# Kernel optimization log

Hardware: AMD Instinct MI355X
Metric: run time of the kernel (lower is better)

Reference implementation:

```python
import jax, jax.numpy as jnp
import numpy as np

B, N, NC = 8, 25200, 80           # YOLOv5-640 / COCO raw output
CONF_THRES = 0.25                  # init conf_threshold
IOU_THRES = 0.45                   # init iou_threshold
PATCH_CONF = 0.001                 # hard-coded patch_conf in forward
GN = jnp.array([640.0, 640.0, 640.0, 640.0], dtype=jnp.float32)  # img_size[[1,0,1,0]]
MAX_WH = 4096.0                    # class offset for class-aware NMS
K_CLEAN = 512                      # fixed-size cap on NMS candidates (clean branch)
K_PATCH = 1024                     # fixed-size cap on NMS candidates (patch branch)
MAX_DET_CLEAN = 1000
MAX_DET_PATCH = 30000
NEG = jnp.float32(-1e30)


def _xywh2xyxy(x):
    xy, wh = x[..., :2], x[..., 2:4]
    return jnp.concatenate([xy - wh * 0.5, xy + wh * 0.5], axis=-1)


def _pairwise_iou(a, b):
    # a: [A,4] xyxy, b: [B,4] xyxy -> [A,B] jaccard overlap
    tl = jnp.maximum(a[:, None, :2], b[None, :, :2])
    br = jnp.minimum(a[:, None, 2:4], b[None, :, 2:4])
    wh = jnp.clip(br - tl, 0.0)
    inter = wh[..., 0] * wh[..., 1]
    area_a = (a[:, 2] - a[:, 0]) * (a[:, 3] - a[:, 1])
    area_b = (b[:, 2] - b[:, 0]) * (b[:, 3] - b[:, 1])
    union = area_a[:, None] + area_b[None, :] - inter
    union = jnp.where(union > 0, union, 1.0)  # guard degenerate boxes
    return inter / union


def _nms_single(pred, conf_thres, K, max_det):
    # pred: [N, 5+nc]. Fixed-size (padded/masked) greedy NMS, class-aware via MAX_WH offset.
    obj = pred[:, 4]
    cls_conf = pred[:, 5:] * obj[:, None]          # x[:,5:] *= x[:,4:5]
    conf = jnp.max(cls_conf, axis=-1)
    cls = jnp.argmax(cls_conf, axis=-1)
    box = _xywh2xyxy(pred[:, :4])
    valid = (obj > conf_thres) & (conf > conf_thres)
    scores = jnp.where(valid, conf, NEG)
    top_scores, idx = jax.lax.top_k(scores, K)     # sorted desc, like torchvision NMS ordering
    boxes = box[idx]
    cls_k = cls[idx]
    valid_k = top_scores > conf_thres
    boxes_off = boxes + cls_k.astype(boxes.dtype)[:, None] * MAX_WH
    iou = jax.lax.stop_gradient(_pairwise_iou(boxes_off, boxes_off))
    ar = jnp.arange(K)

    def step(keep, i):
        sup = keep[i] & (iou[i] > IOU_THRES) & (ar > i)
        return keep & (~sup), None

    keep, _ = jax.lax.scan(step, valid_k, jnp.arange(K))
    rank = jnp.cumsum(keep.astype(jnp.int32))
    keep = keep & (rank <= max_det)
    return boxes, cls_k, keep


def _image_loss(cb, cc, ck, pb, pc, pk):
    # per clean detection: max IoU over kept patch boxes of the same class (0 if none)
    iou = _pairwise_iou(cb / GN, pb / GN)          # [K_CLEAN, K_PATCH]
    mask = ck[:, None] & pk[None, :] & (cc[:, None] == pc[None, :])
    tm = jnp.max(jnp.where(mask, iou, 0.0), axis=1)
    s = jnp.sum(jnp.where(ck, tm, 0.0))
    n = jnp.sum(ck.astype(jnp.float32))
    return s, n


def _forward(output_clean, output_patch):
    cb, cc, ck = jax.vmap(lambda p: _nms_single(p, CONF_THRES, K_CLEAN, MAX_DET_CLEAN))(output_clean)
    pb, pc, pk = jax.vmap(lambda p: _nms_single(p, PATCH_CONF, K_PATCH, MAX_DET_PATCH))(output_patch)
    s, n = jax.vmap(_image_loss)(cb, cc, ck, pb, pc, pk)
    total, cnt = jnp.sum(s), jnp.sum(n)
    return jnp.where(cnt > 0, 1.0 - total / jnp.maximum(cnt, 1.0), jnp.float32(1.0))


def _make_pred(key):
    ka, kb, kc, kd = jax.random.split(key, 4)
    cxcy = jax.random.uniform(ka, (B, N, 2), jnp.float32, 20.0, 620.0)
    wh = jax.random.uniform(kb, (B, N, 2), jnp.float32, 2.0, 150.0)
    obj = jax.random.uniform(kc, (B, N, 1), jnp.float32)
    clsp = jax.random.uniform(kd, (B, N, NC), jnp.float32)
    return jnp.concatenate([cxcy, wh, obj, clsp], axis=-1)


def setup_inputs() -> dict:
    key = jax.random.key(0)
    k1, k2 = jax.random.split(key)
    return {"output_clean": _make_pred(k1), "output_patch": _make_pred(k2)}


def reference(output_clean, output_patch):
    return _forward(output_clean, output_patch)
```

## Files before the change

### kernel.cpp

```cpp
#include <hip/hip_runtime.h>


static constexpr int NB   = 8;
static constexpr int NA   = 25200;
static constexpr int NCLS = 80;
static constexpr int CH   = 85;
static constexpr int NT   = 16;
static constexpr int KMAX = 1024;
static constexpr int NBIN = 32768;
static constexpr int PSH  = 17;
static constexpr int CAP  = 2048;
static constexpr int IOB  = 34;

static constexpr size_t OFF_KEYS = 0;
static constexpr size_t OFF_CLS  = OFF_KEYS + (size_t)NT * NA * 4;
static constexpr size_t OFF_BOX  = OFF_CLS  + (size_t)NT * NA * 4;
static constexpr size_t OFF_CLSK = OFF_BOX  + (size_t)NT * KMAX * 16;
static constexpr size_t OFF_VALK = OFF_CLSK + (size_t)NT * KMAX * 4;
static constexpr size_t OFF_KEEP = OFF_VALK + (size_t)NT * KMAX * 4;
static constexpr size_t OFF_SUP  = OFF_KEEP + (size_t)NT * 16 * 8;
static constexpr size_t OFF_DIAG = OFF_SUP  + (size_t)NT * KMAX * 16 * 8;
static constexpr size_t OFF_PART = OFF_DIAG + (size_t)NT * KMAX * 8;

__device__ __forceinline__ unsigned okey(float f) {
  unsigned u = __float_as_uint(f);
  return (u & 0x80000000u) ? ~u : (u | 0x80000000u);
}

__device__ __forceinline__ unsigned long long shflx64(unsigned long long v, int m) {
  unsigned lo = (unsigned)v, hi = (unsigned)(v >> 32);
  lo = __shfl_xor(lo, m);
  hi = __shfl_xor(hi, m);
  return ((unsigned long long)hi << 32) | lo;
}

__global__ __launch_bounds__(256) void k_score(const float* __restrict__ clean,
                                               const float* __restrict__ patch,
                                               unsigned* __restrict__ keys,
                                               int* __restrict__ clsArr) {
#pragma clang fp contract(off)
  __shared__ float rows[4][16 * CH];
  const int t    = blockIdx.y;
  const int wave = threadIdx.x >> 6;
  const int lane = threadIdx.x & 63;
  const int a0   = blockIdx.x * 64 + wave * 16;
  if (a0 >= NA) return;
  const float conf_th = (t < 8) ? 0.25f : 0.001f;
  const float* __restrict__ src = ((t < 8) ? clean : patch) + (size_t)(t & 7) * NA * CH;
  const float4* g4 = (const float4*)(src + (size_t)a0 * CH);
  float4* rows4 = (float4*)rows[wave];
#pragma unroll
  for (int c = 0; c < 6; ++c) {
    const int i = (c << 6) + lane;
    if (i < 340) {
      __builtin_amdgcn_global_load_lds(
          (const __attribute__((address_space(1))) void*)(g4 + i),
          (__attribute__((address_space(3))) void*)(rows4 + (c << 6)),
          16, 0, 2 );
    }
  }
  asm volatile("s_waitcnt vmcnt(0)" ::: "memory");
  __builtin_amdgcn_sched_barrier(0);

  const int ar = lane >> 2;
  const int q  = lane & 3;
  const float* r = rows[wave] + ar * CH;
  const float obj = r[4];
  const int c0 = q * 20;
  float best = r[5 + c0] * obj;
  int bc = c0;
  for (int c = c0 + 1; c < c0 + 20; ++c) {
    float v = r[5 + c] * obj;
    if (v > best) { best = v; bc = c; }
  }
  {
    float b2 = __shfl_down(best, 2); int c2 = __shfl_down(bc, 2);
    if (b2 > best || (b2 == best && c2 < bc)) { best = b2; bc = c2; }
    float b1 = __shfl_down(best, 1); int c1 = __shfl_down(bc, 1);
    if (b1 > best || (b1 == best && c1 < bc)) { best = b1; bc = c1; }
  }
  if (q == 0) {
    const bool valid = (obj > conf_th) && (best > conf_th);
    const float score = valid ? best : -1e30f;
    const int a = a0 + ar;
    keys[(size_t)t * NA + a]   = okey(score);
    clsArr[(size_t)t * NA + a] = bc;
  }
}

__global__ __launch_bounds__(1024) void k_topsel(const unsigned* __restrict__ keys,
                                                 const int* __restrict__ clsArr,
                                                 const float* __restrict__ clean,
                                                 const float* __restrict__ patch,
                                                 float* __restrict__ boxesK,
                                                 int* __restrict__ clsK,
                                                 int* __restrict__ validK) {
#pragma clang fp contract(off)
  const int t = blockIdx.x;
  const unsigned K = (t < 8) ? 512u : 1024u;
  const float conf_th = (t < 8) ? 0.25f : 0.001f;
  __shared__ unsigned h32[NBIN / 2];
  __shared__ unsigned long long buf[CAP];
  __shared__ unsigned scnt[2];
  __shared__ unsigned wtot[16], wsuf[16];
  __shared__ int s_chunk;
  __shared__ unsigned s_acc, s_B;
  const int tid = threadIdx.x;
  const int lane = tid & 63, wv = tid >> 6;
  for (int i = tid; i < NBIN / 2; i += 1024) h32[i] = 0u;
  for (int i = tid; i < CAP; i += 1024) buf[i] = 0ull;
  if (tid < 2) scnt[tid] = 0u;
  __syncthreads();
  const unsigned INVKEY = okey(-1e30f);
  const unsigned* kv = keys + (size_t)t * NA;
  {
    const uint4* kv4 = (const uint4*)kv;
    unsigned invCnt = 0;
    for (int i = tid; i < NA / 4; i += 1024) {
      uint4 kq = kv4[i];
      unsigned kk[4] = {kq.x, kq.y, kq.z, kq.w};
#pragma unroll
      for (int c = 0; c < 4; ++c) {
        if (kk[c] == INVKEY) {
          ++invCnt;
        } else {
          unsigned b = kk[c] >> PSH;
          atomicAdd(&h32[b >> 1], 1u << ((b & 1) * 16));
        }
      }
    }
    for (int off = 32; off > 0; off >>= 1) invCnt += __shfl_down(invCnt, off);
    if (lane == 0 && invCnt) {
      unsigned b = INVKEY >> PSH;
      atomicAdd(&h32[b >> 1], invCnt << ((b & 1) * 16));
    }
  }
  __syncthreads();
  unsigned cnt_c = 0;
  for (int i = 0; i < 16; ++i) {
    unsigned v = h32[tid * 16 + i];
    cnt_c += (v & 0xFFFFu) + (v >> 16);
  }
  unsigned s = cnt_c;
  for (int off = 1; off < 64; off <<= 1) {
    unsigned v = __shfl_down(s, off);
    if (lane + off < 64) s += v;
  }
  if (lane == 0) wtot[wv] = s;
  __syncthreads();
  if (tid < 16) {
    unsigned acc = 0;
    for (int w2 = 15; w2 > tid; --w2) acc += wtot[w2];
    wsuf[tid] = acc;
  }
  __syncthreads();
  const unsigned suf = s + wsuf[wv];
  if (suf >= K && suf - cnt_c < K) { s_chunk = tid; s_acc = suf - cnt_c; }
  __syncthreads();
  if (tid == 0) {
    unsigned acc = s_acc;
    unsigned res = (unsigned)(s_chunk * 32);
    for (int i = 31; i >= 0; --i) {
      int bb = s_chunk * 32 + i;
      unsigned v = h32[bb >> 1];
      unsigned c2 = (bb & 1) ? (v >> 16) : (v & 0xFFFFu);
      if (acc + c2 >= K) { res = (unsigned)bb; break; }
      acc += c2;
    }
    s_B = res;
  }
  __syncthreads();
  const unsigned B = s_B;
  const unsigned long long lowmask =
      (lane == 0) ? 0ull : (0xFFFFFFFFFFFFFFFFull >> (64 - lane));
  for (int i = tid; i < 25600; i += 1024) {
    const bool inb = (i < NA);
    unsigned key = inb ? kv[i] : 0u;
    unsigned p = key >> PSH;
    const bool hi = inb && (p > B);
    const bool eq = inb && (p == B);
    const unsigned long long item =
        ((unsigned long long)key << 32) | (unsigned)(~(unsigned)i);
    unsigned long long mh = __ballot(hi);
    if (mh) {
      int leader = (int)__ffsll(mh) - 1;
      unsigned base2 = 0;
      if (lane == leader) base2 = atomicAdd(&scnt[0], (unsigned)__popcll(mh));
      base2 = __shfl(base2, leader);
      if (hi) {
        unsigned pos = base2 + (unsigned)__popcll(mh & lowmask);
        if (pos < 1024u) buf[pos] = item;
      }
    }
    unsigned long long me = __ballot(eq);
    if (me) {
      int leader = (int)__ffsll(me) - 1;
      unsigned base2 = 0;
      if (lane == leader) base2 = atomicAdd(&scnt[1], (unsigned)__popcll(me));
      base2 = __shfl(base2, leader);
      if (eq) {
        unsigned pos = base2 + (unsigned)__popcll(me & lowmask);
        if (pos < 1024u) buf[1024 + pos] = item;
      }
    }
  }
  __syncthreads();
  {
    const int e0 = wv * 128 + lane;
    const int e1 = e0 + 64;
    unsigned long long r0 = buf[e0], r1 = buf[e1];
    for (int kk2 = 2; kk2 <= CAP; kk2 <<= 1) {
      for (int j = kk2 >> 1; j > 0; j >>= 1) {
        if (j >= 128) {
          buf[e0] = r0; buf[e1] = r1;
          __syncthreads();
          unsigned long long o0 = buf[e0 ^ j];
          unsigned long long o1 = buf[e1 ^ j];
          const bool mx = (((e0 & kk2) == 0) == ((e0 & j) == 0));
          r0 = mx ? (r0 > o0 ? r0 : o0) : (r0 < o0 ? r0 : o0);
          r1 = mx ? (r1 > o1 ? r1 : o1) : (r1 < o1 ? r1 : o1);
          __syncthreads();
        } else if (j == 64) {
          const bool up = (e0 & kk2) == 0;
          unsigned long long mxv = r0 > r1 ? r0 : r1;
          unsigned long long mnv = r0 > r1 ? r1 : r0;
          r0 = up ? mxv : mnv;
          r1 = up ? mnv : mxv;
        } else {
          unsigned long long o0 = shflx64(r0, j);
          unsigned long long o1 = shflx64(r1, j);
          const bool up0 = (e0 & kk2) == 0;
          const bool up1 = (e1 & kk2) == 0;
          const bool lo  = (lane & j) == 0;
          const bool m0 = (up0 == lo), m1 = (up1 == lo);
          r0 = m0 ? (r0 > o0 ? r0 : o0) : (r0 < o0 ? r0 : o0);
          r1 = m1 ? (r1 > o1 ? r1 : o1) : (r1 < o1 ? r1 : o1);
        }
      }
    }
    buf[e0] = r0; buf[e1] = r1;
  }
  __syncthreads();
  const float* __restrict__ src = ((t < 8) ? clean : patch) + (size_t)(t & 7) * NA * CH;
  const unsigned vkey = okey(conf_th);
  for (int k = tid; k < (int)K; k += 1024) {
    unsigned long long v = buf[k];
    unsigned key = (unsigned)(v >> 32);
    int idx = (int)(~(unsigned)(v & 0xFFFFFFFFull));
    if (idx < 0 || idx >= NA) idx = 0;
    const float* r = src + (size_t)idx * CH;
    float cx = r[0], cy = r[1], w = r[2], h = r[3];
    float hw = w * 0.5f, hh = h * 0.5f;
    float* bo = boxesK + ((size_t)t * KMAX + k) * 4;
    bo[0] = cx - hw; bo[1] = cy - hh; bo[2] = cx + hw; bo[3] = cy + hh;
    clsK[t * KMAX + k]   = clsArr[(size_t)t * NA + idx];
    validK[t * KMAX + k] = (key > vkey) ? 1 : 0;
  }
}

__global__ __launch_bounds__(256) void k_ioumat(const float* __restrict__ boxesK,
                                                const int* __restrict__ clsK,
                                                unsigned long long* __restrict__ sup,
                                                unsigned long long* __restrict__ diag) {
#pragma clang fp contract(off)
  const int t  = blockIdx.y;
  const int K  = (t < 8) ? 512 : 1024;
  const int lw = (t < 8) ? 3 : 4;
  const int nw = 1 << lw;
  const int npair = (nw * (nw + 1)) / 2;
  const int total = npair * 64;
  if (blockIdx.x * 256 >= total) return;
  __shared__ float X1[KMAX + 16], Y1[KMAX + 16], X2[KMAX + 16], Y2[KMAX + 16], AR[KMAX + 16];
  for (int i = threadIdx.x; i < K; i += 256) {
    const float* bo = boxesK + ((size_t)t * KMAX + i) * 4;
    float off = (float)clsK[t * KMAX + i] * 4096.0f;
    float x1 = bo[0] + off, y1 = bo[1] + off, x2 = bo[2] + off, y2 = bo[3] + off;
    const int ip = i + (i >> 6);
    X1[ip] = x1; Y1[ip] = y1; X2[ip] = x2; Y2[ip] = y2;
    AR[ip] = (x2 - x1) * (y2 - y1);
  }
  __syncthreads();
  unsigned long long* supt = sup + (size_t)t * (KMAX * 16);
  for (int widx = blockIdx.x * 256 + threadIdx.x; widx < total; widx += IOB * 256) {
    int p = widx >> 6;
    int row = widx & 63;
    int rb = 0, pr = p;
    while (pr >= nw - rb) { pr -= nw - rb; ++rb; }
    const int wc = rb + pr;
    const int i = rb * 64 + row;
    const int ipi = i + rb;
    const float x1i = X1[ipi], y1i = Y1[ipi], x2i = X2[ipi], y2i = Y2[ipi], ai = AR[ipi];
    unsigned long long m = 0ull;
    const int jb = (wc << 6) + wc;
    const bool offd = (wc > rb);
#pragma unroll 4
    for (int l = 0; l < 64; ++l) {
      const int jp = jb + l;
      float tlx = fmaxf(x1i, X1[jp]);
      float tly = fmaxf(y1i, Y1[jp]);
      float brx = fminf(x2i, X2[jp]);
      float bry = fminf(y2i, Y2[jp]);
      float w = fmaxf(brx - tlx, 0.0f);
      float h = fmaxf(bry - tly, 0.0f);
      float inter = w * h;
      float uni = (ai + AR[jp]) - inter;
      uni = (uni > 0.0f) ? uni : 1.0f;
      float iou = inter / uni;
      bool hit = (iou > 0.45f) && (offd || ((wc << 6) + l > i));
      m |= hit ? (1ull << l) : 0ull;
    }
    supt[(size_t)i * nw + wc] = m;
    if (wc == rb) diag[(size_t)t * KMAX + i] = m;
  }
}

__global__ __launch_bounds__(64) void k_greedy(const unsigned long long* __restrict__ sup,
                                               const unsigned long long* __restrict__ diag,
                                               const int* __restrict__ validK,
                                               unsigned long long* __restrict__ keepw) {
  const int t  = blockIdx.x;
  const int K  = (t < 8) ? 512 : 1024;
  const int lw = (t < 8) ? 3 : 4;
  const int nw = 1 << lw;
  const int lane = threadIdx.x;
  __shared__ unsigned long long sdiag[KMAX];
  const unsigned long long* dg = diag + (size_t)t * KMAX;
  for (int i = lane; i < K; i += 64) sdiag[i] = dg[i];
  int v16[16];
#pragma unroll
  for (int W = 0; W < 16; ++W)
    v16[W] = (W < nw) ? validK[t * KMAX + W * 64 + lane] : 0;
  unsigned long long vkeep = 0ull;
#pragma unroll
  for (int W = 0; W < 16; ++W)
    if (W < nw) {
      unsigned long long bl = __ballot(v16[W] != 0);
      if (lane == W) vkeep = bl;
    }
  __syncthreads();
  const int w = lane & (nw - 1);
  const int b = lane >> lw;
  const int r0 = b * nw;
  const unsigned long long* base = sup + (size_t)t * (KMAX * 16);
  unsigned long long remv = 0ull;
  for (int W = 0; W < nw; ++W) {
    unsigned long long vv[16];
    if (W + 1 < nw) {
#pragma unroll
      for (int j = 0; j < 16; ++j)
        vv[j] = (j < nw) ? base[(size_t)(W * 64 + r0 + j) * nw + w] : 0ull;
    }
    unsigned long long cur = __shfl(vkeep, W) & ~__shfl(remv, W);
    for (int rb = 0; rb < 64; rb += 16) {
      unsigned long long tm[16];
#pragma unroll
      for (int i2 = 0; i2 < 16; ++i2) tm[i2] = sdiag[W * 64 + rb + i2];
#pragma unroll
      for (int i2 = 0; i2 < 16; ++i2) {
        unsigned long long msk = 0ull - ((cur >> (rb + i2)) & 1ull);
        cur &= ~(tm[i2] & msk);
      }
    }
    if (lane == 0) keepw[t * 16 + W] = cur;
    if (W + 1 < nw) {
      unsigned long long part = 0ull;
#pragma unroll
      for (int j = 0; j < 16; ++j) {
        bool take = (j < nw) && (w > W) && ((cur >> (r0 + j)) & 1ull);
        part |= take ? vv[j] : 0ull;
      }
      for (int s = nw; s < 64; s <<= 1) part |= __shfl_xor(part, s);
      remv |= part;
    }
  }
}

__global__ __launch_bounds__(1024) void k_loss(const float* __restrict__ boxesK,
                                               const int* __restrict__ clsK,
                                               const unsigned long long* __restrict__ keepw,
                                               float* __restrict__ part) {
#pragma clang fp contract(off)
  const int img = blockIdx.y;
  const int chunk = blockIdx.x;
  const int tp = 8 + img;
  __shared__ float px1[KMAX], py1[KMAX], px2[KMAX], py2[KMAX], pa[KMAX];
  __shared__ int pcls[KMAX];
  __shared__ float red[1024];
  for (int j = threadIdx.x; j < KMAX; j += 1024) {
    const float* bo = boxesK + ((size_t)tp * KMAX + j) * 4;
    float x1 = bo[0] / 640.0f, y1 = bo[1] / 640.0f;
    float x2 = bo[2] / 640.0f, y2 = bo[3] / 640.0f;
    px1[j] = x1; py1[j] = y1; px2[j] = x2; py2[j] = y2;
    pa[j] = (x2 - x1) * (y2 - y1);
    int kept = (int)((keepw[tp * 16 + (j >> 6)] >> (j & 63)) & 1ull);
    pcls[j] = kept ? clsK[tp * KMAX + j] : -1;
  }
  __syncthreads();
  const int row = chunk * 64 + (threadIdx.x & 63);
  const int stripe = threadIdx.x >> 6;
  const int ck = (int)((keepw[img * 16 + (row >> 6)] >> (row & 63)) & 1ull);
  const float* bo = boxesK + ((size_t)img * KMAX + row) * 4;
  float cx1 = bo[0] / 640.0f, cy1 = bo[1] / 640.0f;
  float cx2 = bo[2] / 640.0f, cy2 = bo[3] / 640.0f;
  float ca = (cx2 - cx1) * (cy2 - cy1);
  const int ccls = clsK[img * KMAX + row];
  float m = 0.0f;
  if (ck) {
    const int j0 = stripe * 64;
    for (int j = j0; j < j0 + 64; ++j) {
      if (pcls[j] == ccls) {
        float tlx = fmaxf(cx1, px1[j]);
        float tly = fmaxf(cy1, py1[j]);
        float brx = fminf(cx2, px2[j]);
        float bry = fminf(cy2, py2[j]);
        float w = fmaxf(brx - tlx, 0.0f);
        float h = fmaxf(bry - tly, 0.0f);
        float inter = w * h;
        float uni = (ca + pa[j]) - inter;
        uni = (uni > 0.0f) ? uni : 1.0f;
        m = fmaxf(m, inter / uni);
      }
    }
  }
  red[threadIdx.x] = m;
  __syncthreads();
  if (threadIdx.x < 64) {
    float mm = red[threadIdx.x];
#pragma unroll
    for (int s = 1; s < 16; ++s) mm = fmaxf(mm, red[threadIdx.x + 64 * s]);
    float sv = ck ? mm : 0.0f;
    float nv = ck ? 1.0f : 0.0f;
    for (int off = 32; off > 0; off >>= 1) {
      sv += __shfl_down(sv, off);
      nv += __shfl_down(nv, off);
    }
    if (threadIdx.x == 0) {
      int b = img * 8 + chunk;
      part[b * 2 + 0] = sv;
      part[b * 2 + 1] = nv;
    }
  }
}

__global__ __launch_bounds__(64) void k_final(const float* __restrict__ part,
                                              float* __restrict__ out) {
  int lane = threadIdx.x;
  float sv = part[lane * 2 + 0];
  float nv = part[lane * 2 + 1];
  for (int off = 32; off > 0; off >>= 1) {
    sv += __shfl_down(sv, off);
    nv += __shfl_down(nv, off);
  }
  if (lane == 0) out[0] = (nv > 0.0f) ? (1.0f - sv / fmaxf(nv, 1.0f)) : 1.0f;
}

extern "C" void kernel_launch(void* const* d_in, const int* in_sizes, int n_in,
                              void* d_out, int out_size, void* d_ws, size_t ws_size,
                              hipStream_t stream) {
  const float* clean = (const float*)d_in[0];
  const float* patch = (const float*)d_in[1];
  char* ws = (char*)d_ws;
  unsigned* keys            = (unsigned*)(ws + OFF_KEYS);
  int* clsArr               = (int*)(ws + OFF_CLS);
  float* boxesK             = (float*)(ws + OFF_BOX);
  int* clsK                 = (int*)(ws + OFF_CLSK);
  int* validK               = (int*)(ws + OFF_VALK);
  unsigned long long* keepw = (unsigned long long*)(ws + OFF_KEEP);
  unsigned long long* sup   = (unsigned long long*)(ws + OFF_SUP);
  unsigned long long* diag  = (unsigned long long*)(ws + OFF_DIAG);
  float* part               = (float*)(ws + OFF_PART);
  float* out                = (float*)d_out;

  k_score  <<<dim3((NA + 63) / 64, NT), 256, 0, stream>>>(clean, patch, keys, clsArr);
  k_topsel <<<NT, 1024, 0, stream>>>(keys, clsArr, clean, patch, boxesK, clsK, validK);
  k_ioumat <<<dim3(IOB, NT), 256, 0, stream>>>(boxesK, clsK, sup, diag);
  k_greedy <<<NT, 64, 0, stream>>>(sup, diag, validK, keepw);
  k_loss   <<<dim3(8, NB), 1024, 0, stream>>>(boxesK, clsK, keepw, part);
  k_final  <<<1, 64, 0, stream>>>(part, out);
}
```

Before: 247.9 us.

## Build score histogram with global atomics in scoring kernel instead of top-select

Moves the per-task radix histogram construction out of the single-block-per-task top-select kernel and into the massively parallel scoring kernel, which now does global atomic adds into a workspace histogram zeroed by a new kernel. The top-select kernel loads its histogram slice into registers, finds the threshold bin without shared memory, and keeps the keys in registers for the compaction pass instead of reading them again. This removes the serial shared-memory histogram phase done by only 16 blocks. In exchange it adds a zeroing launch, global atomic contention on hot bins (the invalid-key bin is aggregated per wave), and higher register pressure.

```diff
diff --git a/kernel.cpp b/kernel.cpp
--- a/kernel.cpp
+++ b/kernel.cpp
@@ -21,6 +21,7 @@
 static constexpr size_t OFF_SUP  = OFF_KEEP + (size_t)NT * 16 * 8;
 static constexpr size_t OFF_DIAG = OFF_SUP  + (size_t)NT * KMAX * 16 * 8;
 static constexpr size_t OFF_PART = OFF_DIAG + (size_t)NT * KMAX * 8;
+static constexpr size_t OFF_HIST = OFF_PART + 512;
 
 __device__ __forceinline__ unsigned okey(float f) {
   unsigned u = __float_as_uint(f);
@@ -34,10 +35,15 @@
   return ((unsigned long long)hi << 32) | lo;
 }
 
+__global__ __launch_bounds__(256) void k_zero(uint4* __restrict__ hist4) {
+  hist4[blockIdx.x * 256 + threadIdx.x] = make_uint4(0u, 0u, 0u, 0u);
+}
+
 __global__ __launch_bounds__(256) void k_score(const float* __restrict__ clean,
                                                const float* __restrict__ patch,
                                                unsigned* __restrict__ keys,
-                                               int* __restrict__ clsArr) {
+                                               int* __restrict__ clsArr,
+                                               unsigned* __restrict__ hist) {
 #pragma clang fp contract(off)
   __shared__ float rows[4][16 * CH];
   const int t    = blockIdx.y;
@@ -82,9 +88,18 @@
   if (q == 0) {
     const bool valid = (obj > conf_th) && (best > conf_th);
     const float score = valid ? best : -1e30f;
+    const unsigned key = okey(score);
     const int a = a0 + ar;
-    keys[(size_t)t * NA + a]   = okey(score);
+    keys[(size_t)t * NA + a]   = key;
     clsArr[(size_t)t * NA + a] = bc;
+    unsigned* ht = hist + (size_t)t * NBIN;
+    if (valid) {
+      atomicAdd(&ht[key >> PSH], 1u);
+    } else {
+      unsigned long long mb = __ballot(true);
+      if (lane == (int)__ffsll(mb) - 1)
+        atomicAdd(&ht[okey(-1e30f) >> PSH], (unsigned)__popcll(mb));
+    }
   }
 }
 
@@ -92,6 +107,7 @@
                                                  const int* __restrict__ clsArr,
                                                  const float* __restrict__ clean,
                                                  const float* __restrict__ patch,
+                                                 const unsigned* __restrict__ hist,
                                                  float* __restrict__ boxesK,
                                                  int* __restrict__ clsK,
                                                  int* __restrict__ validK) {
@@ -99,48 +115,35 @@
   const int t = blockIdx.x;
   const unsigned K = (t < 8) ? 512u : 1024u;
   const float conf_th = (t < 8) ? 0.25f : 0.001f;
-  __shared__ unsigned h32[NBIN / 2];
   __shared__ unsigned long long buf[CAP];
   __shared__ unsigned scnt[2];
   __shared__ unsigned wtot[16], wsuf[16];
-  __shared__ int s_chunk;
-  __shared__ unsigned s_acc, s_B;
+  __shared__ unsigned s_B;
   const int tid = threadIdx.x;
   const int lane = tid & 63, wv = tid >> 6;
-  for (int i = tid; i < NBIN / 2; i += 1024) h32[i] = 0u;
   for (int i = tid; i < CAP; i += 1024) buf[i] = 0ull;
   if (tid < 2) scnt[tid] = 0u;
-  __syncthreads();
-  const unsigned INVKEY = okey(-1e30f);
   const unsigned* kv = keys + (size_t)t * NA;
+  const uint4* kv4 = (const uint4*)kv;
+  uint4 u[7];
+#pragma unroll
+  for (int c = 0; c < 7; ++c) {
+    const int i4 = c * 1024 + tid;
+    if (i4 < NA / 4) u[c] = kv4[i4];
+    else { u[c].x = 0u; u[c].y = 0u; u[c].z = 0u; u[c].w = 0u; }
+  }
+  unsigned hb[32];
   {
-    const uint4* kv4 = (const uint4*)kv;
-    unsigned invCnt = 0;
-    for (int i = tid; i < NA / 4; i += 1024) {
-      uint4 kq = kv4[i];
-      unsigned kk[4] = {kq.x, kq.y, kq.z, kq.w};
-#pragma unroll
-      for (int c = 0; c < 4; ++c) {
-        if (kk[c] == INVKEY) {
-          ++invCnt;
-        } else {
-          unsigned b = kk[c] >> PSH;
-          atomicAdd(&h32[b >> 1], 1u << ((b & 1) * 16));
-        }
-      }
-    }
-    for (int off = 32; off > 0; off >>= 1) invCnt += __shfl_down(invCnt, off);
-    if (lane == 0 && invCnt) {
-      unsigned b = INVKEY >> PSH;
-      atomicAdd(&h32[b >> 1], invCnt << ((b & 1) * 16));
-    }
-  }
-  __syncthreads();
+    const uint4* gh4 = (const uint4*)(hist + (size_t)t * NBIN + (size_t)tid * 32);
+#pragma unroll
+    for (int i = 0; i < 8; ++i) {
+      uint4 h4 = gh4[i];
+      hb[i * 4 + 0] = h4.x; hb[i * 4 + 1] = h4.y; hb[i * 4 + 2] = h4.z; hb[i * 4 + 3] = h4.w;
+    }
+  }
   unsigned cnt_c = 0;
-  for (int i = 0; i < 16; ++i) {
-    unsigned v = h32[tid * 16 + i];
-    cnt_c += (v & 0xFFFFu) + (v >> 16);
-  }
+#pragma unroll
+  for (int i = 0; i < 32; ++i) cnt_c += hb[i];
   unsigned s = cnt_c;
   for (int off = 1; off < 64; off <<= 1) {
     unsigned v = __shfl_down(s, off);
@@ -155,17 +158,17 @@
   }
   __syncthreads();
   const unsigned suf = s + wsuf[wv];
-  if (suf >= K && suf - cnt_c < K) { s_chunk = tid; s_acc = suf - cnt_c; }
-  __syncthreads();
-  if (tid == 0) {
-    unsigned acc = s_acc;
-    unsigned res = (unsigned)(s_chunk * 32);
+  if (suf >= K && suf - cnt_c < K) {
+    unsigned acc = suf - cnt_c;
+    unsigned res = (unsigned)(tid * 32);
+    bool found = false;
+#pragma unroll
     for (int i = 31; i >= 0; --i) {
-      int bb = s_chunk * 32 + i;
-      unsigned v = h32[bb >> 1];
-      unsigned c2 = (bb & 1) ? (v >> 16) : (v & 0xFFFFu);
-      if (acc + c2 >= K) { res = (unsigned)bb; break; }
-      acc += c2;
+      const unsigned c2 = hb[i];
+      if (!found) {
+        if (acc + c2 >= K) { res = (unsigned)(tid * 32 + i); found = true; }
+        else acc += c2;
+      }
     }
     s_B = res;
   }
@@ -173,34 +176,41 @@
   const unsigned B = s_B;
   const unsigned long long lowmask =
       (lane == 0) ? 0ull : (0xFFFFFFFFFFFFFFFFull >> (64 - lane));
-  for (int i = tid; i < 25600; i += 1024) {
-    const bool inb = (i < NA);
-    unsigned key = inb ? kv[i] : 0u;
-    unsigned p = key >> PSH;
-    const bool hi = inb && (p > B);
-    const bool eq = inb && (p == B);
-    const unsigned long long item =
-        ((unsigned long long)key << 32) | (unsigned)(~(unsigned)i);
-    unsigned long long mh = __ballot(hi);
-    if (mh) {
-      int leader = (int)__ffsll(mh) - 1;
-      unsigned base2 = 0;
-      if (lane == leader) base2 = atomicAdd(&scnt[0], (unsigned)__popcll(mh));
-      base2 = __shfl(base2, leader);
-      if (hi) {
-        unsigned pos = base2 + (unsigned)__popcll(mh & lowmask);
-        if (pos < 1024u) buf[pos] = item;
-      }
-    }
-    unsigned long long me = __ballot(eq);
-    if (me) {
-      int leader = (int)__ffsll(me) - 1;
-      unsigned base2 = 0;
-      if (lane == leader) base2 = atomicAdd(&scnt[1], (unsigned)__popcll(me));
-      base2 = __shfl(base2, leader);
-      if (eq) {
-        unsigned pos = base2 + (unsigned)__popcll(me & lowmask);
-        if (pos < 1024u) buf[1024 + pos] = item;
+#pragma unroll
+  for (int c = 0; c < 7; ++c) {
+    const int i4 = c * 1024 + tid;
+    const bool inb = (i4 < NA / 4);
+    unsigned kk[4] = {u[c].x, u[c].y, u[c].z, u[c].w};
+#pragma unroll
+    for (int e = 0; e < 4; ++e) {
+      const unsigned key = kk[e];
+      const unsigned p = key >> PSH;
+      const bool hi = inb && (p > B);
+      const bool eq = inb && (p == B);
+      const int idx = i4 * 4 + e;
+      const unsigned long long item =
+          ((unsigned long long)key << 32) | (unsigned)(~(unsigned)idx);
+      unsigned long long mh = __ballot(hi);
+      if (mh) {
+        int leader = (int)__ffsll(mh) - 1;
+        unsigned base2 = 0;
+        if (lane == leader) base2 = atomicAdd(&scnt[0], (unsigned)__popcll(mh));
+        base2 = __shfl(base2, leader);
+        if (hi) {
+          unsigned pos = base2 + (unsigned)__popcll(mh & lowmask);
+          if (pos < 1024u) buf[pos] = item;
+        }
+      }
+      unsigned long long me = __ballot(eq);
+      if (me) {
+        int leader = (int)__ffsll(me) - 1;
+        unsigned base2 = 0;
+        if (lane == leader) base2 = atomicAdd(&scnt[1], (unsigned)__popcll(me));
+        base2 = __shfl(base2, leader);
+        if (eq) {
+          unsigned pos = base2 + (unsigned)__popcll(me & lowmask);
+          if (pos < 1024u) buf[1024 + pos] = item;
+        }
       }
     }
   }
@@ -469,10 +479,12 @@
   unsigned long long* sup   = (unsigned long long*)(ws + OFF_SUP);
   unsigned long long* diag  = (unsigned long long*)(ws + OFF_DIAG);
   float* part               = (float*)(ws + OFF_PART);
+  unsigned* hist            = (unsigned*)(ws + OFF_HIST);
   float* out                = (float*)d_out;
 
-  k_score  <<<dim3((NA + 63) / 64, NT), 256, 0, stream>>>(clean, patch, keys, clsArr);
-  k_topsel <<<NT, 1024, 0, stream>>>(keys, clsArr, clean, patch, boxesK, clsK, validK);
+  k_zero   <<<(NT * NBIN * 4) / (16 * 256), 256, 0, stream>>>((uint4*)hist);
+  k_score  <<<dim3((NA + 63) / 64, NT), 256, 0, stream>>>(clean, patch, keys, clsArr, hist);
+  k_topsel <<<NT, 1024, 0, stream>>>(keys, clsArr, clean, patch, hist, boxesK, clsK, validK);
   k_ioumat <<<dim3(IOB, NT), 256, 0, stream>>>(boxesK, clsK, sup, diag);
   k_greedy <<<NT, 64, 0, stream>>>(sup, diag, validK, keepw);
   k_loss   <<<dim3(8, NB), 1024, 0, stream>>>(boxesK, clsK, keepw, part);
```

Measured after the change: 316.5 us. 1.28x slower.

## Fuse final reduction into loss kernel and double rows per scoring wave

Applied to the files above, without the earlier changes.

The final reduction kernel is removed. The last k_loss block to finish, detected through an atomic counter that k_score resets, now performs the 64-way reduction and writes the output, saving one kernel launch. k_score also processes 32 anchors per wave instead of 16, with two lanes per anchor scanning 40 classes each, which halves the grid size and doubles the LDS staging per wave. The costs are longer serial argmax loops per lane and reliance on threadfence and atomic ordering for correctness.

```diff
diff --git a/kernel.cpp b/kernel.cpp
--- a/kernel.cpp
+++ b/kernel.cpp
@@ -21,6 +21,7 @@
 static constexpr size_t OFF_SUP  = OFF_KEEP + (size_t)NT * 16 * 8;
 static constexpr size_t OFF_DIAG = OFF_SUP  + (size_t)NT * KMAX * 16 * 8;
 static constexpr size_t OFF_PART = OFF_DIAG + (size_t)NT * KMAX * 8;
+static constexpr size_t OFF_CNT  = OFF_PART + 512;
 
 __device__ __forceinline__ unsigned okey(float f) {
   unsigned u = __float_as_uint(f);
@@ -37,22 +38,26 @@
 __global__ __launch_bounds__(256) void k_score(const float* __restrict__ clean,
                                                const float* __restrict__ patch,
                                                unsigned* __restrict__ keys,
-                                               int* __restrict__ clsArr) {
+                                               int* __restrict__ clsArr,
+                                               unsigned* __restrict__ cnt) {
 #pragma clang fp contract(off)
-  __shared__ float rows[4][16 * CH];
+  if (blockIdx.x == 0 && blockIdx.y == 0 && threadIdx.x == 0) *cnt = 0u;
+  __shared__ float rows[4][32 * CH];
   const int t    = blockIdx.y;
   const int wave = threadIdx.x >> 6;
   const int lane = threadIdx.x & 63;
-  const int a0   = blockIdx.x * 64 + wave * 16;
+  const int a0   = blockIdx.x * 128 + wave * 32;
   if (a0 >= NA) return;
+  const int nA = (NA - a0 < 32) ? (NA - a0) : 32;
   const float conf_th = (t < 8) ? 0.25f : 0.001f;
   const float* __restrict__ src = ((t < 8) ? clean : patch) + (size_t)(t & 7) * NA * CH;
   const float4* g4 = (const float4*)(src + (size_t)a0 * CH);
   float4* rows4 = (float4*)rows[wave];
-#pragma unroll
-  for (int c = 0; c < 6; ++c) {
+  const int n4 = (nA * CH) >> 2;
+#pragma unroll
+  for (int c = 0; c < 11; ++c) {
     const int i = (c << 6) + lane;
-    if (i < 340) {
+    if (i < n4) {
       __builtin_amdgcn_global_load_lds(
           (const __attribute__((address_space(1))) void*)(g4 + i),
           (__attribute__((address_space(3))) void*)(rows4 + (c << 6)),
@@ -62,29 +67,27 @@
   asm volatile("s_waitcnt vmcnt(0)" ::: "memory");
   __builtin_amdgcn_sched_barrier(0);
 
-  const int ar = lane >> 2;
-  const int q  = lane & 3;
-  const float* r = rows[wave] + ar * CH;
-  const float obj = r[4];
-  const int c0 = q * 20;
-  float best = r[5 + c0] * obj;
-  int bc = c0;
-  for (int c = c0 + 1; c < c0 + 20; ++c) {
-    float v = r[5 + c] * obj;
-    if (v > best) { best = v; bc = c; }
-  }
-  {
-    float b2 = __shfl_down(best, 2); int c2 = __shfl_down(bc, 2);
-    if (b2 > best || (b2 == best && c2 < bc)) { best = b2; bc = c2; }
+  const int ar = lane >> 1;
+  const int q  = lane & 1;
+  if (ar < nA) {
+    const float* r = rows[wave] + ar * CH;
+    const float obj = r[4];
+    const int c0 = q * 40;
+    float best = r[5 + c0] * obj;
+    int bc = c0;
+    for (int c = c0 + 1; c < c0 + 40; ++c) {
+      float v = r[5 + c] * obj;
+      if (v > best) { best = v; bc = c; }
+    }
     float b1 = __shfl_down(best, 1); int c1 = __shfl_down(bc, 1);
     if (b1 > best || (b1 == best && c1 < bc)) { best = b1; bc = c1; }
-  }
-  if (q == 0) {
-    const bool valid = (obj > conf_th) && (best > conf_th);
-    const float score = valid ? best : -1e30f;
-    const int a = a0 + ar;
-    keys[(size_t)t * NA + a]   = okey(score);
-    clsArr[(size_t)t * NA + a] = bc;
+    if (q == 0) {
+      const bool valid = (obj > conf_th) && (best > conf_th);
+      const float score = valid ? best : -1e30f;
+      const int a = a0 + ar;
+      keys[(size_t)t * NA + a]   = okey(score);
+      clsArr[(size_t)t * NA + a] = bc;
+    }
   }
 }
 
@@ -378,7 +381,9 @@
 __global__ __launch_bounds__(1024) void k_loss(const float* __restrict__ boxesK,
                                                const int* __restrict__ clsK,
                                                const unsigned long long* __restrict__ keepw,
-                                               float* __restrict__ part) {
+                                               float* __restrict__ part,
+                                               unsigned* __restrict__ cnt,
+                                               float* __restrict__ out) {
 #pragma clang fp contract(off)
   const int img = blockIdx.y;
   const int chunk = blockIdx.x;
@@ -386,6 +391,7 @@
   __shared__ float px1[KMAX], py1[KMAX], px2[KMAX], py2[KMAX], pa[KMAX];
   __shared__ int pcls[KMAX];
   __shared__ float red[1024];
+  __shared__ unsigned s_last;
   for (int j = threadIdx.x; j < KMAX; j += 1024) {
     const float* bo = boxesK + ((size_t)tp * KMAX + j) * 4;
     float x1 = bo[0] / 640.0f, y1 = bo[1] / 640.0f;
@@ -438,20 +444,23 @@
       int b = img * 8 + chunk;
       part[b * 2 + 0] = sv;
       part[b * 2 + 1] = nv;
-    }
-  }
-}
-
-__global__ __launch_bounds__(64) void k_final(const float* __restrict__ part,
-                                              float* __restrict__ out) {
-  int lane = threadIdx.x;
-  float sv = part[lane * 2 + 0];
-  float nv = part[lane * 2 + 1];
-  for (int off = 32; off > 0; off >>= 1) {
-    sv += __shfl_down(sv, off);
-    nv += __shfl_down(nv, off);
-  }
-  if (lane == 0) out[0] = (nv > 0.0f) ? (1.0f - sv / fmaxf(nv, 1.0f)) : 1.0f;
+      __threadfence();
+      unsigned old = atomicAdd(cnt, 1u);
+      s_last = (old == 63u) ? 1u : 0u;
+    }
+  }
+  __syncthreads();
+  if (s_last && threadIdx.x < 64) {
+    __threadfence();
+    volatile const float* vp = part;
+    float sv = vp[threadIdx.x * 2 + 0];
+    float nv = vp[threadIdx.x * 2 + 1];
+    for (int off = 32; off > 0; off >>= 1) {
+      sv += __shfl_down(sv, off);
+      nv += __shfl_down(nv, off);
+    }
+    if (threadIdx.x == 0) out[0] = (nv > 0.0f) ? (1.0f - sv / fmaxf(nv, 1.0f)) : 1.0f;
+  }
 }
 
 extern "C" void kernel_launch(void* const* d_in, const int* in_sizes, int n_in,
@@ -469,12 +478,12 @@
   unsigned long long* sup   = (unsigned long long*)(ws + OFF_SUP);
   unsigned long long* diag  = (unsigned long long*)(ws + OFF_DIAG);
   float* part               = (float*)(ws + OFF_PART);
+  unsigned* cnt             = (unsigned*)(ws + OFF_CNT);
   float* out                = (float*)d_out;
 
-  k_score  <<<dim3((NA + 63) / 64, NT), 256, 0, stream>>>(clean, patch, keys, clsArr);
+  k_score  <<<dim3((NA + 127) / 128, NT), 256, 0, stream>>>(clean, patch, keys, clsArr, cnt);
   k_topsel <<<NT, 1024, 0, stream>>>(keys, clsArr, clean, patch, boxesK, clsK, validK);
   k_ioumat <<<dim3(IOB, NT), 256, 0, stream>>>(boxesK, clsK, sup, diag);
   k_greedy <<<NT, 64, 0, stream>>>(sup, diag, validK, keepw);
-  k_loss   <<<dim3(8, NB), 1024, 0, stream>>>(boxesK, clsK, keepw, part);
-  k_final  <<<1, 64, 0, stream>>>(part, out);
-}
+  k_loss   <<<dim3(8, NB), 1024, 0, stream>>>(boxesK, clsK, keepw, part, cnt, out);
+}
```

Result: no change. 249.9 us (median of 2 runs) (+0.8%).
